# Optimization experiments

Hardware: AMD Instinct MI355X
Metric: run time of the kernel (lower is better)

The kernel has to match this reference:

```python
import jax, jax.numpy as jnp
import numpy as np

B, N, C = 4, 2304, 256
H = 8                      # num_heads
D = C // H                 # head_dim = 32
SCALE = D ** -0.5
H_DS, W_DS = 48, 48
UP = 2                     # spatial_down_ratio
EPS = 1e-5


def setup_inputs() -> dict:
    key = jax.random.key(0)
    ks = jax.random.split(key, 16)
    g = lambda k, shape, s: (jax.random.normal(k, shape, dtype=jnp.float32) * s)
    return {
        "x1": g(ks[0], (B, N, C), 1.0),
        "x2": g(ks[1], (B, N, C), 1.0),
        # attention projections (torch Linear convention: [out, in], no bias)
        "q1_w": g(ks[2], (C, C), C ** -0.5),
        "kv1_w": g(ks[3], (2 * C, C), C ** -0.5),
        "q2_w": g(ks[4], (C, C), C ** -0.5),
        "kv2_w": g(ks[5], (2 * C, C), C ** -0.5),
        # per-head scalar biases
        "beta12": jnp.full((H,), 0.2, dtype=jnp.float32),
        "beta21": jnp.full((H,), 0.1, dtype=jnp.float32),
        # output projections
        "p1_w": g(ks[6], (C, C), (2.0 / C) ** 0.5),
        "p1_b": g(ks[7], (C,), 1e-2),
        "p2_w": g(ks[8], (C, C), (2.0 / C) ** 0.5),
        "p2_b": g(ks[9], (C,), 1e-2),
        # LayerNorm affine params
        "g1": jnp.ones((C,), dtype=jnp.float32),
        "b1": jnp.zeros((C,), dtype=jnp.float32),
        "g2": jnp.ones((C,), dtype=jnp.float32),
        "b2": jnp.zeros((C,), dtype=jnp.float32),
    }


def _heads(x):
    # [B,N,C] -> [B,H,N,D]
    return x.reshape(B, N, H, D).transpose(0, 2, 1, 3)


def _merge(x):
    # [B,H,N,D] -> [B,N,C]
    return x.transpose(0, 2, 1, 3).reshape(B, N, C)


def _cross_attn(q, k, v, beta):
    # scores: [B,H,N,N] with per-head scalar bias
    s = jnp.einsum("bhqd,bhkd->bhqk", q, k) * SCALE + beta[None, :, None, None]
    a = jax.nn.softmax(s, axis=-1)
    return jnp.einsum("bhqk,bhkd->bhqd", a, v)


def _layernorm(x, g, b):
    mu = jnp.mean(x, axis=-1, keepdims=True)
    var = jnp.var(x, axis=-1, keepdims=True)
    return (x - mu) * jax.lax.rsqrt(var + EPS) * g + b


def _forward(x1, x2, q1_w, kv1_w, q2_w, kv2_w, beta12, beta21,
             p1_w, p1_b, p2_w, p2_b, g1, b1, g2, b2):
    q1 = _heads(x1 @ q1_w.T)
    kv1 = x1 @ kv1_w.T          # [B,N,2C]
    k1, v1 = _heads(kv1[..., :C]), _heads(kv1[..., C:])
    q2 = _heads(x2 @ q2_w.T)
    kv2 = x2 @ kv2_w.T
    k2, v2 = _heads(kv2[..., :C]), _heads(kv2[..., C:])

    o1 = _merge(_cross_attn(q1, k2, v2, beta12))   # x1 attends to x2
    o2 = _merge(_cross_attn(q2, k1, v1, beta21))   # x2 attends to x1

    y1 = _layernorm(jax.nn.relu(o1 @ p1_w.T + p1_b), g1, b1)
    y2 = _layernorm(jax.nn.relu(o2 @ p2_w.T + p2_b), g2, b2)

    # [B,N,C] -> [B,C,H_ds,W_ds]
    y1 = y1.transpose(0, 2, 1).reshape(B, C, H_DS, W_DS)
    y2 = y2.transpose(0, 2, 1).reshape(B, C, H_DS, W_DS)

    # bilinear upsample x2, align_corners=False (half-pixel == jax.image default)
    out_shape = (B, C, H_DS * UP, W_DS * UP)
    y1 = jax.image.resize(y1, out_shape, method="bilinear")
    y2 = jax.image.resize(y2, out_shape, method="bilinear")
    return y1, y2


def reference(x1, x2, q1_w, kv1_w, q2_w, kv2_w, beta12, beta21,
              p1_w, p1_b, p2_w, p2_b, g1, b1, g2, b2):
    return _forward(x1, x2, q1_w, kv1_w, q2_w, kv2_w, beta12, beta21,
                    p1_w, p1_b, p2_w, p2_b, g1, b1, g2, b2)
```

## Files before the change

### kernel.cpp

```cpp
#include <hip/hip_runtime.h>
#include <math.h>


typedef __attribute__((ext_vector_type(8))) short short8;
typedef __attribute__((ext_vector_type(4))) float f32x4;

#define MFMA16(a, b, c) __builtin_amdgcn_mfma_f32_16x16x32_bf16((a), (b), (c), 0, 0, 0)

__device__ __forceinline__ float bf2f(ushort u) {
    union { unsigned u; float f; } x; x.u = ((unsigned)u) << 16; return x.f;
}
__device__ __forceinline__ ushort f2bf(float f) {
    union { float f; unsigned u; } x; x.f = f;
    unsigned u = x.u;
    return (ushort)((u + 0x7fffu + ((u >> 16) & 1u)) >> 16);
}
__device__ __forceinline__ unsigned cvt_pk_bf16(float a, float b) {
    unsigned r;
    asm("v_cvt_pk_bf16_f32 %0, %1, %2" : "=v"(r) : "v"(a), "v"(b));
    return r;
}

__global__ void sniff_kernel(const ushort* __restrict__ x, int* __restrict__ flag)
{
    int lane = threadIdx.x;
    ushort u = x[lane * 2];
    int e = (u >> 7) & 0xFF;
    int outlier = (e < 100 || e > 135) ? 1 : 0;
    unsigned long long m = __ballot(outlier);
    if (lane == 0) *flag = (__popcll(m) >= 16) ? 1 : 0;
}

__global__ __launch_bounds__(256) void convert_params(
    const void* s0, const void* s1, const void* s2, const void* s3,
    const void* s4, const void* s5, const void* s6, const void* s7,
    const void* s8, const void* s9, const void* s10, const void* s11,
    ushort* __restrict__ dst, const int* __restrict__ flag)
{
    int idx = blockIdx.x * 256 + threadIdx.x;
    if (idx >= 525824) return;
    const void* src; int off;
    if      (idx < 65536)  { src = s0;  off = idx; }
    else if (idx < 196608) { src = s1;  off = idx - 65536; }
    else if (idx < 262144) { src = s2;  off = idx - 196608; }
    else if (idx < 393216) { src = s3;  off = idx - 262144; }
    else if (idx < 458752) { src = s4;  off = idx - 393216; }
    else if (idx < 524288) { src = s5;  off = idx - 458752; }
    else if (idx < 524544) { src = s6;  off = idx - 524288; }
    else if (idx < 524800) { src = s7;  off = idx - 524544; }
    else if (idx < 525056) { src = s8;  off = idx - 524800; }
    else if (idx < 525312) { src = s9;  off = idx - 525056; }
    else if (idx < 525568) { src = s10; off = idx - 525312; }
    else                   { src = s11; off = idx - 525568; }
    ushort v = (*flag) ? f2bf(((const float*)src)[off])
                       : ((const ushort*)src)[off];
    dst[idx] = v;
}

__global__ __launch_bounds__(256) void convert_x(
    const void* __restrict__ x1, const void* __restrict__ x2,
    ushort* __restrict__ o1, ushort* __restrict__ o2,
    const int* __restrict__ flag)
{
    int idx = blockIdx.x * 256 + threadIdx.x;
    int which = idx >= 294912;
    int off = (which ? idx - 294912 : idx) * 8;
    const void* src = which ? x2 : x1;
    ushort* dst = which ? o2 : o1;
    if (*flag) {
        const float* p = (const float*)src + off;
        float4 a = *(const float4*)p;
        float4 c = *(const float4*)(p + 4);
        uint4 u;
        u.x = cvt_pk_bf16(a.x, a.y);
        u.y = cvt_pk_bf16(a.z, a.w);
        u.z = cvt_pk_bf16(c.x, c.y);
        u.w = cvt_pk_bf16(c.z, c.w);
        *(uint4*)(dst + off) = u;
    } else {
        *(uint4*)(dst + off) = *(const uint4*)((const ushort*)src + off);
    }
}

__global__ __launch_bounds__(256) void gemm_bt(
    const void* __restrict__ Ain, const ushort* __restrict__ W,
    ushort* __restrict__ C, const ushort* __restrict__ bias,
    int M, int N, int K, int relu, const int* __restrict__ dflag, int a_ext,
    int mode, ushort* __restrict__ Kh, ushort* __restrict__ Vt,
    const ushort* __restrict__ W2, const ushort* __restrict__ bias2,
    ushort* __restrict__ Kh2, ushort* __restrict__ Vt2, int mhalf)
{
    __shared__ __align__(16) ushort As[64][40];
    __shared__ __align__(16) ushort Ws[64][40];

    const int m0 = blockIdx.x * 64;
    const int n0 = blockIdx.y * 64;
    const int tid = threadIdx.x;
    const int w = tid >> 6;
    const int lane = tid & 63;
    const int lm = lane & 15;
    const int quad = lane >> 4;
    const int a32 = a_ext ? *dflag : 0;

    const int side = (mhalf && m0 >= mhalf) ? 1 : 0;
    const ushort* Wu = side ? W2 : W;
    const ushort* bu = side ? bias2 : bias;
    ushort* Khu = side ? Kh2 : Kh;
    ushort* Vtu = side ? Vt2 : Vt;

    const f32x4 Z4 = {0.f, 0.f, 0.f, 0.f};
    f32x4 acc[4];
    for (int j = 0; j < 4; j++) acc[j] = Z4;

    const ushort* A16 = (const ushort*)Ain;
    const float*  A32 = (const float*)Ain;
    const int row = tid >> 2, off = (tid & 3) * 8;

    for (int k0 = 0; k0 < K; k0 += 32) {
        __syncthreads();
        if (a32) {
            const float* p0 = A32 + (size_t)(m0 + row) * K + k0 + off;
            float4 f0 = *(const float4*)p0;
            float4 f1 = *(const float4*)(p0 + 4);
            uint4 t0;
            t0.x = cvt_pk_bf16(f0.x, f0.y);
            t0.y = cvt_pk_bf16(f0.z, f0.w);
            t0.z = cvt_pk_bf16(f1.x, f1.y);
            t0.w = cvt_pk_bf16(f1.z, f1.w);
            *(uint4*)&As[row][off] = t0;
        } else {
            *(uint4*)&As[row][off] =
                *(const uint4*)(A16 + (size_t)(m0 + row) * K + k0 + off);
        }
        *(uint4*)&Ws[row][off] =
            *(const uint4*)(Wu + (size_t)(n0 + row) * K + k0 + off);
        __syncthreads();

        short8 af = *(const short8*)&As[w * 16 + lm][quad * 8];
        for (int nt = 0; nt < 4; nt++) {
            short8 wf = *(const short8*)&Ws[nt * 16 + lm][quad * 8];
            acc[nt] = MFMA16(af, wf, acc[nt]);
        }
    }

    const int grow = m0 + w * 16 + quad * 4;
    const int grel = grow - (side ? mhalf : 0);
    if (mode == 1) {
        const float QSC = 0.17677669529663687f * 1.4426950408889634f;
        int bb = grel / 2304;
        int tok = grel - bb * 2304;
        for (int nt = 0; nt < 4; nt++) {
            int col = n0 + nt * 16 + lm;
            if (col < 256) {
                for (int r = 0; r < 4; r++)
                    C[(size_t)(grow + r) * 256 + col] = f2bf(acc[nt][r] * QSC);
            } else if (col < 512) {
                int c2 = col - 256, hh = c2 >> 5, d = c2 & 31;
                for (int r = 0; r < 4; r++)
                    Khu[(((size_t)bb * 8 + hh) * 2304 + tok + r) * 32 + d] = f2bf(acc[nt][r]);
            } else {
                int c2 = col - 512, hh = c2 >> 5, d = c2 & 31;
                uint2 o;
                o.x = cvt_pk_bf16(acc[nt][0], acc[nt][1]);
                o.y = cvt_pk_bf16(acc[nt][2], acc[nt][3]);
                *(uint2*)&Vtu[(((size_t)bb * 8 + hh) * 32 + d) * 2304 + tok] = o;
            }
        }
    } else {
        for (int nt = 0; nt < 4; nt++) {
            int col = n0 + nt * 16 + lm;
            float bv = bu ? bf2f(bu[col]) : 0.f;
            for (int r = 0; r < 4; r++) {
                float v = acc[nt][r] + bv;
                if (relu) v = fmaxf(v, 0.f);
                C[(size_t)(grow + r) * N + col] = f2bf(v);
            }
        }
    }
}

__global__ __launch_bounds__(256) void attn_kernel(
    const ushort* __restrict__ Qa, const ushort* __restrict__ Kha,
    const ushort* __restrict__ Vta, ushort* __restrict__ Oa,
    const ushort* __restrict__ Qb, const ushort* __restrict__ Khb2,
    const ushort* __restrict__ Vtb2, ushort* __restrict__ Ob)
{
    __shared__ __align__(16) ushort Ksh[64][40];
    __shared__ __align__(16) ushort Vsh[32][72];
    __shared__ __align__(16) ushort Pl[4][16][80];

    const int qb = blockIdx.x;
    const int side = blockIdx.y >> 5;
    const int bh = blockIdx.y & 31;
    const ushort* Q  = side ? Qb   : Qa;
    const ushort* Kh = side ? Khb2 : Kha;
    const ushort* Vt = side ? Vtb2 : Vta;
    ushort* O        = side ? Ob   : Oa;

    const int b = bh >> 3;
    const int tid = threadIdx.x;
    const int w = tid >> 6, lane = tid & 63;
    const int lm = lane & 15, quad = lane >> 4;
    const f32x4 Z4 = {0.f, 0.f, 0.f, 0.f};

    const int qrow = qb * 64 + w * 16 + lm;
    const int h = bh & 7;
    short8 qf = *(const short8*)(Q + ((size_t)b * 2304 + qrow) * 256 + h * 32 + quad * 8);

    f32x4 o_acc[2]; o_acc[0] = Z4; o_acc[1] = Z4;
    float l = 0.f;

    const ushort* Khb = Kh + (size_t)bh * 2304 * 32;
    const ushort* Vtb = Vt + (size_t)bh * 32 * 2304;
    const int ks_row = tid >> 2, ks_off = (tid & 3) * 8;
    const int vs_row = tid >> 3, vs_off = (tid & 7) * 8;

    const ushort* kptr = Khb + (size_t)ks_row * 32 + ks_off;
    const ushort* vptr = Vtb + (size_t)vs_row * 2304 + vs_off;
    uint4 kreg = *(const uint4*)kptr;
    uint4 vreg = *(const uint4*)vptr;

    for (int kc = 0; kc < 36; kc++) {
        __syncthreads();
        *(uint4*)&Ksh[ks_row][ks_off] = kreg;
        *(uint4*)&Vsh[vs_row][vs_off] = vreg;
        __syncthreads();

        int nk = kc < 35 ? kc + 1 : 35;
        kreg = *(const uint4*)(kptr + (size_t)nk * 2048);
        vreg = *(const uint4*)(vptr + nk * 64);

        f32x4 s[4];
        for (int t = 0; t < 4; t++) {
            short8 kf = *(const short8*)&Ksh[t * 16 + lm][quad * 8];
            s[t] = MFMA16(kf, qf, Z4);
        }

        for (int t = 0; t < 4; t++) {
            float p0 = exp2f(s[t][0]);
            float p1 = exp2f(s[t][1]);
            float p2 = exp2f(s[t][2]);
            float p3 = exp2f(s[t][3]);
            l += (p0 + p1) + (p2 + p3);
            uint2 pk;
            pk.x = cvt_pk_bf16(p0, p1);
            pk.y = cvt_pk_bf16(p2, p3);
            *(uint2*)&Pl[w][lm][t * 16 + quad * 4] = pk;
        }
        asm volatile("s_waitcnt lgkmcnt(0)" ::: "memory");

        for (int g = 0; g < 2; g++) {
            short8 pf = *(const short8*)&Pl[w][lm][g * 32 + quad * 8];
            for (int dt = 0; dt < 2; dt++) {
                short8 vf = *(const short8*)&Vsh[dt * 16 + lm][g * 32 + quad * 8];
                o_acc[dt] = MFMA16(vf, pf, o_acc[dt]);
            }
        }
    }

    l += __shfl_xor(l, 16, 64);
    l += __shfl_xor(l, 32, 64);
    float rl = 1.f / l;
    for (int dt = 0; dt < 2; dt++) {
        uint2 o;
        o.x = cvt_pk_bf16(o_acc[dt][0] * rl, o_acc[dt][1] * rl);
        o.y = cvt_pk_bf16(o_acc[dt][2] * rl, o_acc[dt][3] * rl);
        *(uint2*)(O + ((size_t)b * 2304 + qrow) * 256 + h * 32 + dt * 16 + quad * 4)
            = o;
    }
}

__global__ __launch_bounds__(256) void lnt_kernel(
    const ushort* __restrict__ Z, const ushort* __restrict__ G1,
    const ushort* __restrict__ B1, const ushort* __restrict__ G2,
    const ushort* __restrict__ B2, ushort* __restrict__ Yt)
{
    __shared__ ushort T[256][72];

    const int tid = threadIdx.x;
    const int tok0 = blockIdx.x * 32;
    const int half = (tok0 >= 9216) ? 1 : 0;
    const int tr = tok0 - half * 9216;
    const int bb = tr / 2304;
    const int tokb = tr - bb * 2304;

    const int tok_l = tid >> 3;
    const int cq = tid & 7;

    const ushort* zp = Z + ((size_t)(tok0 + tok_l)) * 256 + cq * 32;
    uint dd[16];
    for (int i = 0; i < 4; i++) {
        uint4 v = *(const uint4*)(zp + i * 8);
        dd[i * 4 + 0] = v.x; dd[i * 4 + 1] = v.y;
        dd[i * 4 + 2] = v.z; dd[i * 4 + 3] = v.w;
    }
    float s = 0.f, q = 0.f;
    for (int e = 0; e < 16; e++) {
        float x0 = bf2f((ushort)dd[e]);
        float x1 = bf2f((ushort)(dd[e] >> 16));
        s += x0 + x1;
        q += x0 * x0 + x1 * x1;
    }
    s += __shfl_xor(s, 1, 64); q += __shfl_xor(q, 1, 64);
    s += __shfl_xor(s, 2, 64); q += __shfl_xor(q, 2, 64);
    s += __shfl_xor(s, 4, 64); q += __shfl_xor(q, 4, 64);
    float mu = s * (1.f / 256.f);
    float var = q * (1.f / 256.f) - mu * mu;
    float rs = rsqrtf(var + 1e-5f);

    const ushort* Gs = half ? G2 : G1;
    const ushort* Bs = half ? B2 : B1;
    const int col = tok_l + 4 * cq;

    for (int i = 0; i < 4; i++) {
        int cb = cq * 32 + i * 8;
        uint4 gv = *(const uint4*)(Gs + cb);
        uint4 bv = *(const uint4*)(Bs + cb);
        uint gg[4] = {gv.x, gv.y, gv.z, gv.w};
        uint bw[4] = {bv.x, bv.y, bv.z, bv.w};
        for (int k = 0; k < 4; k++) {
            uint u = dd[i * 4 + k];
            float x0 = bf2f((ushort)u), x1 = bf2f((ushort)(u >> 16));
            float y0 = (x0 - mu) * rs * bf2f((ushort)gg[k]) + bf2f((ushort)bw[k]);
            float y1 = (x1 - mu) * rs * bf2f((ushort)(gg[k] >> 16))
                     + bf2f((ushort)(bw[k] >> 16));
            int c = cb + 2 * k;
            T[c][col]     = f2bf(y0);
            T[c + 1][col] = f2bf(y1);
        }
    }
    __syncthreads();

    const int c_row = tid >> 3;
    const int tq = (tid & 7) * 4;
    const size_t obase = ((size_t)((half * 4 + bb) * 256)) * 2304 + tokb + tq;
    for (int i = 0; i < 8; i++) {
        int c = c_row + 32 * i;
        uint2 v = *(const uint2*)&T[c][tq + 4 * i];
        *(uint2*)(Yt + obase + (size_t)c * 2304) = v;
    }
}

__global__ __launch_bounds__(256) void upsample_kernel(
    const ushort* __restrict__ Yt, float* __restrict__ out)
{
    int idx = blockIdx.x * 256 + threadIdx.x;
    int m  = idx % 48;
    int t  = idx / 48;
    int oi = t % 96;
    int bc = t / 96;

    float fi = oi * 0.5f - 0.25f;
    int i0 = (int)floorf(fi);
    float wi = fi - (float)i0;
    int i1 = i0 + 1 < 47 ? i0 + 1 : 47;
    i0 = i0 > 0 ? i0 : 0;
    int jm = m - 1 > 0 ? m - 1 : 0;
    int jp = m + 1 < 47 ? m + 1 : 47;

    const ushort* r0 = Yt + (size_t)bc * 2304 + i0 * 48;
    const ushort* r1 = Yt + (size_t)bc * 2304 + i1 * 48;
    float a0 = bf2f(r0[jm]), b0 = bf2f(r0[m]), c0 = bf2f(r0[jp]);
    float a1 = bf2f(r1[jm]), b1 = bf2f(r1[m]), c1 = bf2f(r1[jp]);
    float u = 1.f - wi;
    float ha = u * a0 + wi * a1;
    float hb = u * b0 + wi * b1;
    float hc = u * c0 + wi * c1;
    float2 o;
    o.x = 0.25f * ha + 0.75f * hb;
    o.y = 0.75f * hb + 0.25f * hc;
    *(float2*)(out + (size_t)bc * 9216 + oi * 96 + m * 2) = o;
}

extern "C" void kernel_launch(void* const* d_in, const int* in_sizes, int n_in,
                              void* d_out, int out_size, void* d_ws, size_t ws_size,
                              hipStream_t stream)
{
    (void)in_sizes; (void)n_in; (void)out_size; (void)ws_size;

    ushort* ws  = (ushort*)d_ws;
    ushort* Q1  = ws;
    ushort* Q2  = Q1  + 2359296;
    ushort* KV1 = Q2  + 2359296;
    ushort* KV2 = KV1 + 4718592;
    ushort* wc  = KV2 + 4718592;
    int*    dflag = (int*)(wc + 525824);

    ushort* cqkv1w = wc;
    ushort* cqkv2w = wc + 196608;
    ushort* cp1w  = wc + 393216;
    ushort* cp2w  = wc + 458752;
    ushort* cp1b  = wc + 524288;
    ushort* cp2b  = wc + 524544;
    ushort* cg1   = wc + 524800;
    ushort* cb1   = wc + 525056;
    ushort* cg2   = wc + 525312;
    ushort* cb2   = wc + 525568;

    float*  outf = (float*)d_out;
    ushort* O1  = (ushort*)d_out;
    ushort* O2  = O1 + 2359296;
    ushort* Xb1 = O2 + 2359296;
    ushort* Xb2 = Xb1 + 2359296;
    ushort* Z1  = KV2;
    ushort* Yt  = Q1;
    (void)Q2; (void)O2; (void)Xb2;

    dim3 blk(256);
    sniff_kernel<<<dim3(1), dim3(64), 0, stream>>>((const ushort*)d_in[0], dflag);
    convert_params<<<dim3(2054), blk, 0, stream>>>(
        d_in[2], d_in[3], d_in[4], d_in[5], d_in[8], d_in[10],
        d_in[9], d_in[11], d_in[12], d_in[13], d_in[14], d_in[15],
        wc, dflag);
    convert_x<<<dim3(2304), blk, 0, stream>>>(d_in[0], d_in[1], Xb1, Xb2, dflag);

    gemm_bt<<<dim3(288, 12), blk, 0, stream>>>(Xb1, cqkv1w, Q1, nullptr,
        18432, 768, 256, 0, dflag, 0, 1, KV1, KV1 + 2359296,
        cqkv2w, nullptr, KV2, KV2 + 2359296, 9216);

    attn_kernel<<<dim3(36, 64), blk, 0, stream>>>(
        Q1, KV2, KV2 + 2359296, O1,
        Q2, KV1, KV1 + 2359296, O2);

    gemm_bt<<<dim3(288, 4), blk, 0, stream>>>(O1, cp1w, Z1, cp1b,
        18432, 256, 256, 1, dflag, 0, 0, nullptr, nullptr,
        cp2w, cp2b, nullptr, nullptr, 9216);

    lnt_kernel<<<dim3(576), blk, 0, stream>>>(Z1, cg1, cb1, cg2, cb2, Yt);

    upsample_kernel<<<dim3(36864), blk, 0, stream>>>(Yt, outf);
}
```

Before: 295.5 us.

## Switch attention to 32x32 MFMA with register-resident P via permlane swap

The attention kernel now uses 32x32x16 bf16 MFMA tiles, so each wave handles 32 query rows and each block 128, which halves the grid. The softmax probabilities are repacked between lanes with permlane32_swap so they feed the PV MFMA straight from registers, removing the shared-memory P buffer round trip and its wait. The larger tile reuses each K/V chunk across more queries, but it raises register pressure and the halved grid (1152 blocks) may reduce occupancy.

```diff
diff --git a/kernel.cpp b/kernel.cpp
--- a/kernel.cpp
+++ b/kernel.cpp
@@ -4,8 +4,11 @@
 
 typedef __attribute__((ext_vector_type(8))) short short8;
 typedef __attribute__((ext_vector_type(4))) float f32x4;
+typedef __attribute__((ext_vector_type(16))) float f32x16;
+typedef __attribute__((ext_vector_type(2))) unsigned uint32x2;
 
 #define MFMA16(a, b, c) __builtin_amdgcn_mfma_f32_16x16x32_bf16((a), (b), (c), 0, 0, 0)
+#define MFMA32(a, b, c) __builtin_amdgcn_mfma_f32_32x32x16_bf16((a), (b), (c), 0, 0, 0)
 
 __device__ __forceinline__ float bf2f(ushort u) {
     union { unsigned u; float f; } x; x.u = ((unsigned)u) << 16; return x.f;
@@ -19,6 +22,10 @@
     unsigned r;
     asm("v_cvt_pk_bf16_f32 %0, %1, %2" : "=v"(r) : "v"(a), "v"(b));
     return r;
+}
+__device__ __forceinline__ void plswap(unsigned &a, unsigned &b) {
+    uint32x2 r = __builtin_amdgcn_permlane32_swap(a, b, false, false);
+    a = r[0]; b = r[1];
 }
 
 __global__ void sniff_kernel(const ushort* __restrict__ x, int* __restrict__ flag)
@@ -187,7 +194,6 @@
 {
     __shared__ __align__(16) ushort Ksh[64][40];
     __shared__ __align__(16) ushort Vsh[32][72];
-    __shared__ __align__(16) ushort Pl[4][16][80];
 
     const int qb = blockIdx.x;
     const int side = blockIdx.y >> 5;
@@ -197,17 +203,20 @@
     const ushort* Vt = side ? Vtb2 : Vta;
     ushort* O        = side ? Ob   : Oa;
 
-    const int b = bh >> 3;
+    const int b = bh >> 3, h = bh & 7;
     const int tid = threadIdx.x;
     const int w = tid >> 6, lane = tid & 63;
-    const int lm = lane & 15, quad = lane >> 4;
-    const f32x4 Z4 = {0.f, 0.f, 0.f, 0.f};
-
-    const int qrow = qb * 64 + w * 16 + lm;
-    const int h = bh & 7;
-    short8 qf = *(const short8*)(Q + ((size_t)b * 2304 + qrow) * 256 + h * 32 + quad * 8);
-
-    f32x4 o_acc[2]; o_acc[0] = Z4; o_acc[1] = Z4;
+    const int l31 = lane & 31, hl = lane >> 5;
+
+    const int qrow = qb * 128 + w * 32 + l31;
+    const ushort* qp = Q + ((size_t)b * 2304 + qrow) * 256 + h * 32 + hl * 8;
+    short8 qf0 = *(const short8*)qp;
+    short8 qf1 = *(const short8*)(qp + 16);
+
+    f32x16 o_acc;
+    #pragma unroll
+    for (int i = 0; i < 16; i++) o_acc[i] = 0.f;
+    const f32x16 Z16 = o_acc;
     float l = 0.f;
 
     const ushort* Khb = Kh + (size_t)bh * 2304 * 32;
@@ -230,43 +239,52 @@
         kreg = *(const uint4*)(kptr + (size_t)nk * 2048);
         vreg = *(const uint4*)(vptr + nk * 64);
 
-        f32x4 s[4];
-        for (int t = 0; t < 4; t++) {
-            short8 kf = *(const short8*)&Ksh[t * 16 + lm][quad * 8];
-            s[t] = MFMA16(kf, qf, Z4);
-        }
-
-        for (int t = 0; t < 4; t++) {
-            float p0 = exp2f(s[t][0]);
-            float p1 = exp2f(s[t][1]);
-            float p2 = exp2f(s[t][2]);
-            float p3 = exp2f(s[t][3]);
-            l += (p0 + p1) + (p2 + p3);
-            uint2 pk;
-            pk.x = cvt_pk_bf16(p0, p1);
-            pk.y = cvt_pk_bf16(p2, p3);
-            *(uint2*)&Pl[w][lm][t * 16 + quad * 4] = pk;
-        }
-        asm volatile("s_waitcnt lgkmcnt(0)" ::: "memory");
-
-        for (int g = 0; g < 2; g++) {
-            short8 pf = *(const short8*)&Pl[w][lm][g * 32 + quad * 8];
-            for (int dt = 0; dt < 2; dt++) {
-                short8 vf = *(const short8*)&Vsh[dt * 16 + lm][g * 32 + quad * 8];
-                o_acc[dt] = MFMA16(vf, pf, o_acc[dt]);
-            }
-        }
-    }
-
-    l += __shfl_xor(l, 16, 64);
+        #pragma unroll
+        for (int t = 0; t < 2; t++) {
+            short8 kf0 = *(const short8*)&Ksh[t * 32 + l31][hl * 8];
+            short8 kf1 = *(const short8*)&Ksh[t * 32 + l31][16 + hl * 8];
+            f32x16 s = MFMA32(kf0, qf0, Z16);
+            s = MFMA32(kf1, qf1, s);
+
+            float p[16];
+            #pragma unroll
+            for (int i = 0; i < 16; i++) p[i] = exp2f(s[i]);
+            l += (((p[0] + p[1]) + (p[2] + p[3])) + ((p[4] + p[5]) + (p[6] + p[7])))
+               + (((p[8] + p[9]) + (p[10] + p[11])) + ((p[12] + p[13]) + (p[14] + p[15])));
+
+            unsigned c0 = cvt_pk_bf16(p[0],  p[1]);
+            unsigned c1 = cvt_pk_bf16(p[2],  p[3]);
+            unsigned c2 = cvt_pk_bf16(p[4],  p[5]);
+            unsigned c3 = cvt_pk_bf16(p[6],  p[7]);
+            unsigned c4 = cvt_pk_bf16(p[8],  p[9]);
+            unsigned c5 = cvt_pk_bf16(p[10], p[11]);
+            unsigned c6 = cvt_pk_bf16(p[12], p[13]);
+            unsigned c7 = cvt_pk_bf16(p[14], p[15]);
+            plswap(c0, c2);
+            plswap(c1, c3);
+            plswap(c4, c6);
+            plswap(c5, c7);
+
+            union { unsigned u[4]; short8 s8; } pA, pB;
+            pA.u[0] = c0; pA.u[1] = c1; pA.u[2] = c2; pA.u[3] = c3;
+            pB.u[0] = c4; pB.u[1] = c5; pB.u[2] = c6; pB.u[3] = c7;
+
+            short8 vf0 = *(const short8*)&Vsh[l31][t * 32 + hl * 8];
+            short8 vf1 = *(const short8*)&Vsh[l31][t * 32 + 16 + hl * 8];
+            o_acc = MFMA32(vf0, pA.s8, o_acc);
+            o_acc = MFMA32(vf1, pB.s8, o_acc);
+        }
+    }
+
     l += __shfl_xor(l, 32, 64);
     float rl = 1.f / l;
-    for (int dt = 0; dt < 2; dt++) {
+    ushort* op = O + ((size_t)b * 2304 + qrow) * 256 + h * 32 + hl * 4;
+    #pragma unroll
+    for (int g = 0; g < 4; g++) {
         uint2 o;
-        o.x = cvt_pk_bf16(o_acc[dt][0] * rl, o_acc[dt][1] * rl);
-        o.y = cvt_pk_bf16(o_acc[dt][2] * rl, o_acc[dt][3] * rl);
-        *(uint2*)(O + ((size_t)b * 2304 + qrow) * 256 + h * 32 + dt * 16 + quad * 4)
-            = o;
+        o.x = cvt_pk_bf16(o_acc[4 * g] * rl, o_acc[4 * g + 1] * rl);
+        o.y = cvt_pk_bf16(o_acc[4 * g + 2] * rl, o_acc[4 * g + 3] * rl);
+        *(uint2*)(op + 8 * g) = o;
     }
 }
 
@@ -418,7 +436,7 @@
         18432, 768, 256, 0, dflag, 0, 1, KV1, KV1 + 2359296,
         cqkv2w, nullptr, KV2, KV2 + 2359296, 9216);
 
-    attn_kernel<<<dim3(36, 64), blk, 0, stream>>>(
+    attn_kernel<<<dim3(18, 64), blk, 0, stream>>>(
         Q1, KV2, KV2 + 2359296, O1,
         Q2, KV1, KV1 + 2359296, O2);
 
```

Result: no change. 292.1 us (-1.2%).
